# Kernel optimization log

Measured on AMD Instinct MI355X. Metric: run time of the kernel, lower is better.

## Reference

```python
import jax, jax.numpy as jnp
import numpy as np

EMB_DIM, D_H, BSZ, SEQ = 2048, 128, 4, 4096
HALF = D_H // 2


def apply_rope(x, sin, cos):
    # x: [b, s, d]; sin/cos: [s, d//2]; interleaved-pair rotation
    b, s, d = x.shape
    xr = x.reshape(b, s, d // 2, 2)
    x0, x1 = xr[..., 0], xr[..., 1]
    r0 = x0 * cos - x1 * sin
    r1 = x1 * cos + x0 * sin
    return jnp.stack([r0, r1], axis=-1).reshape(b, s, d)


def setup_inputs() -> dict:
    key = jax.random.key(0)
    kx, kq, kk, kv = jax.random.split(key, 4)
    x = jax.random.normal(kx, (BSZ, SEQ, EMB_DIM), dtype=jnp.float32)
    # causal mask (1 = attend, 0 = masked), matching mask[q,:] slicing in source
    mask = jnp.tril(jnp.ones((SEQ, SEQ), dtype=jnp.int32))
    # standard RoPE angle tables: [seq, d_h//2]
    inv_freq = 1.0 / (10000.0 ** (jnp.arange(HALF, dtype=jnp.float32) / HALF))
    angles = jnp.arange(SEQ, dtype=jnp.float32)[:, None] * inv_freq[None, :]
    sin, cos = jnp.sin(angles), jnp.cos(angles)
    scale = 1.0 / np.sqrt(EMB_DIM)
    W_Q = jax.random.normal(kq, (EMB_DIM, D_H), dtype=jnp.float32) * scale
    W_K = jax.random.normal(kk, (EMB_DIM, D_H), dtype=jnp.float32) * scale
    W_V = jax.random.normal(kv, (EMB_DIM, D_H), dtype=jnp.float32) * scale
    return {"x": x, "mask": mask, "sin": sin, "cos": cos,
            "W_Q": W_Q, "W_K": W_K, "W_V": W_V}


def reference(x, mask, sin, cos, W_Q, W_V, W_K):
    # QKV projections
    Q = apply_rope(x @ W_Q, sin, cos)  # [b, s, d_h]
    K = apply_rope(x @ W_K, sin, cos)  # [b, s, d_h]
    V = x @ W_V                        # [b, s, d_h]
    # The source's chunked loop is exactly full masked attention over all K/V.
    scores = jnp.einsum('bqd,bkd->bqk', Q, K) / jnp.sqrt(jnp.float32(D_H))
    scores = jnp.where(mask[None, :, :] == 0, -jnp.inf, scores)
    attn = jax.nn.softmax(scores, axis=-1)
    return jnp.einsum('bqk,bkd->bqd', attn, V)
```

## Files before the change

kernel.cpp:

```cpp
#include <hip/hip_runtime.h>
#include <stdint.h>
#include <stddef.h>

typedef __bf16 bf16;
typedef __bf16 bf16x8 __attribute__((ext_vector_type(8)));
typedef float f32x4 __attribute__((ext_vector_type(4)));
typedef unsigned int uint32x2 __attribute__((ext_vector_type(2)));
typedef unsigned int uint32x4 __attribute__((ext_vector_type(4)));

typedef const __attribute__((address_space(1))) uint32_t GU32;
typedef __attribute__((address_space(3))) uint32_t LU32;

__device__ __forceinline__ f32x4 mfma16(bf16x8 a, bf16x8 b, f32x4 c) {
  return __builtin_amdgcn_mfma_f32_16x16x32_bf16(a, b, c, 0, 0, 0);
}
__device__ __forceinline__ void gload16(const void* g, void* l) {
  __builtin_amdgcn_global_load_lds((GU32*)g, (LU32*)l, 16, 0, 0);
}

__global__ __launch_bounds__(256) void k_prep(const float* __restrict__ Wq,
                                              const float* __restrict__ Wk,
                                              const float* __restrict__ Wv,
                                              bf16* __restrict__ Wct) {
  __shared__ float tile[64][65];
  const int tid = threadIdx.x;
  const int widx = blockIdx.x >> 6, rem = blockIdx.x & 63;
  const int k0 = (rem >> 1) * 64, n0 = (rem & 1) * 64;
  const float* W = (widx == 0) ? Wq : (widx == 1) ? Wk : Wv;
  const int rg = tid >> 4, cq = tid & 15;
#pragma unroll
  for (int i = 0; i < 4; ++i) {
    int krow = i * 16 + rg;
    f32x4 v = *(const f32x4*)(W + (size_t)(k0 + krow) * 128 + n0 + cq * 4);
#pragma unroll
    for (int j = 0; j < 4; ++j) tile[krow][cq * 4 + j] = v[j];
  }
  __syncthreads();
#pragma unroll
  for (int i = 0; i < 4; ++i) {
    int nrow = i * 16 + rg;
    union { bf16 h[4]; uint32x2 u; } pk;
#pragma unroll
    for (int j = 0; j < 4; ++j) pk.h[j] = (bf16)tile[cq * 4 + j][nrow];
    *(uint32x2*)(Wct + (size_t)(widx * 128 + n0 + nrow) * 2048 + k0 + cq * 4) = pk.u;
  }
}

__global__ __launch_bounds__(512, 1) void k_proj(
    const float* __restrict__ x, const float* __restrict__ sint, const float* __restrict__ cost,
    const bf16* __restrict__ Wct, bf16* __restrict__ Qg, bf16* __restrict__ Kg,
    bf16* __restrict__ Vtg) {
  __shared__ __align__(16) uint8_t smem[114688];
  const int tid = threadIdx.x;
  const int lane = tid & 63, w = tid >> 6;
  const int l15 = lane & 15, l16 = lane >> 4;
  const int mb = blockIdx.x;
  const int arow = tid >> 3, aj = tid & 7;

  f32x4 acc[4][3] = {};
  f32x4 regA[2], regB[2];
  uint32x4 br[6];

  const float* abase = x + (size_t)(mb * 64 + arow) * 2048 + aj * 8;

  auto stageB_load = [&](int ks) {
    int k0 = ks * 64;
#pragma unroll
    for (int i = 0; i < 6; ++i) {
      int L = i * 8192 + tid * 16;
      int n = L >> 7, gp = (L >> 4) & 7;
      int cc = gp ^ (n & 7);
      br[i] = *(const uint32x4*)((const uint8_t*)Wct + (((size_t)n * 2048 + k0 + cc * 8) << 1));
    }
  };
  auto stageB_write = [&](int buf) {
    uint8_t* bbm = smem + 16384 + buf * 49152;
#pragma unroll
    for (int i = 0; i < 6; ++i)
      *(uint32x4*)(bbm + i * 8192 + tid * 16) = br[i];
  };
  auto loadA = [&](int ks, f32x4* r) {
    const f32x4* p = (const f32x4*)(abase + ks * 64);
    r[0] = p[0];
    r[1] = p[1];
  };
  auto writeA = [&](int buf, const f32x4* r) {
    uint8_t* ab = smem + buf * 8192;
    union { bf16 v[8]; uint32x4 u; } pk;
#pragma unroll
    for (int e = 0; e < 8; ++e) pk.v[e] = (bf16)r[e >> 2][e & 3];
    *(uint32x4*)(ab + arow * 128 + (((aj ^ (arow & 7)) & 7) << 4)) = pk.u;
  };
  auto compute = [&](int buf) {
    uint8_t* ab = smem + buf * 8192;
    uint8_t* bbm = smem + 16384 + buf * 49152;
    bf16x8 af[2][4], bv[2][3];
#pragma unroll
    for (int kk = 0; kk < 2; ++kk) {
#pragma unroll
      for (int mt = 0; mt < 4; ++mt) {
        int ml = mt * 16 + l15;
        af[kk][mt] = *(const bf16x8*)(ab + ml * 128 + (((kk * 4 + l16) ^ (ml & 7)) << 4));
      }
#pragma unroll
      for (int nt = 0; nt < 3; ++nt) {
        int nl = w * 48 + nt * 16 + l15;
        bv[kk][nt] = *(const bf16x8*)(bbm + nl * 128 + (((kk * 4 + l16) ^ (nl & 7)) << 4));
      }
    }
    __builtin_amdgcn_s_setprio(1);
#pragma unroll
    for (int kk = 0; kk < 2; ++kk)
#pragma unroll
      for (int mt = 0; mt < 4; ++mt)
#pragma unroll
        for (int nt = 0; nt < 3; ++nt)
          acc[mt][nt] = mfma16(af[kk][mt], bv[kk][nt], acc[mt][nt]);
    __builtin_amdgcn_s_setprio(0);
  };

  loadA(0, regA);
  stageB_load(0);
  loadA(1, regB);
  stageB_write(0);
  writeA(0, regA);
  __syncthreads();

  for (int ks = 0; ks < 32; ks += 2) {
    {
      if (ks + 1 < 32) stageB_load(ks + 1);
      if (ks + 2 < 32) loadA(ks + 2, regA);
      compute(0);
      if (ks + 1 < 32) { stageB_write(1); writeA(1, regB); }
      __syncthreads();
    }
    if (ks + 1 < 32) {
      if (ks + 2 < 32) { stageB_load(ks + 2); loadA(ks + 3, regB); }
      compute(1);
      if (ks + 2 < 32) { stageB_write(0); writeA(0, regA); }
      __syncthreads();
    }
  }

  const int bb = mb >> 6;
#pragma unroll
  for (int mt = 0; mt < 4; ++mt) {
    int gm = mb * 64 + mt * 16 + l16 * 4;
    int s0 = gm & 4095;
#pragma unroll
    for (int nt = 0; nt < 3; ++nt) {
      int jcol = w * 48 + nt * 16 + l15;
      f32x4 v = acc[mt][nt];
      if (jcol < 256) {
        int p = (jcol & 127) >> 1;
        bool even = ((jcol & 1) == 0);
#pragma unroll
        for (int r = 0; r < 4; ++r) {
          float pv = __shfl_xor(v[r], 1);
          int s = s0 + r;
          float cs = cost[s * 64 + p], sn = sint[s * 64 + p];
          float nv = even ? (v[r] * cs - pv * sn) : (v[r] * cs + pv * sn);
          bf16 hb = (bf16)nv;
          if (jcol < 128) Qg[((size_t)(bb << 12) + s) * 128 + jcol] = hb;
          else            Kg[((size_t)(bb << 12) + s) * 128 + jcol - 128] = hb;
        }
      } else {
        int d = jcol - 256;
        union { bf16 h[4]; uint32x2 u; } pk;
#pragma unroll
        for (int r = 0; r < 4; ++r) pk.h[r] = (bf16)v[r];
        *(uint32x2*)((uint8_t*)Vtg + (((size_t)(bb << 7) + d) * 4096 + s0) * 2) = pk.u;
      }
    }
  }
}

__global__ __launch_bounds__(256, 2) void k_attn(
    const bf16* __restrict__ Qg, const bf16* __restrict__ Kg, const bf16* __restrict__ Vtg,
    float* __restrict__ PO, float* __restrict__ ML) {
  __shared__ __align__(16) uint8_t smem[81920];
  const int tid = threadIdx.x;
  const int lane = tid & 63, w = tid >> 6;
  const int l15 = lane & 15, l16 = lane >> 4;

  int gid = blockIdx.x;
  int b = gid / 80, rr = gid % 80;
  int j, c;
  if (rr < 8)       { j = rr;                 c = 0; }
  else if (rr < 24) { j = 8 + ((rr - 8) >> 1);  c = (rr - 8) & 1; }
  else if (rr < 48) { j = 16 + (rr - 24) / 3;   c = (rr - 24) % 3; }
  else              { j = 24 + ((rr - 48) >> 2); c = (rr - 48) & 3; }

  const int q0w = j * 128 + w * 32;
  const int kv_lo = c * 1024;
  const int kv_hi = min((c + 1) * 1024, (j + 1) * 128);
  const int T = (kv_hi - kv_lo) >> 6;

  bf16x8 qf[2][4];
#pragma unroll
  for (int qt = 0; qt < 2; ++qt)
#pragma unroll
    for (int kk = 0; kk < 4; ++kk)
      qf[qt][kk] = *(const bf16x8*)(Qg + ((size_t)(b << 12) + q0w + qt * 16 + l15) * 128 + kk * 32 + l16 * 8);

  f32x4 o[2][8] = {};
  float m_r[2] = {-1e30f, -1e30f};
  float l_r[2] = {0.f, 0.f};
  uint8_t* pb = smem + 65536 + w * 4096;

  auto stage = [&](int t) {
    uint8_t* kb = smem + (t & 1) * 32768;
    uint8_t* vb = kb + 16384;
    int kv0 = kv_lo + t * 64;
#pragma unroll
    for (int i = 0; i < 4; ++i) {
      int L = i * 4096 + tid * 16;
      {
        int kv = L >> 8, cp = (L >> 4) & 15, cc = cp ^ (kv & 7);
        const uint8_t* src = (const uint8_t*)Kg + ((size_t)((b << 12) + kv0 + kv) << 8) + (cc << 4);
        gload16(src, kb + i * 4096 + w * 1024);
      }
      {
        int d = L >> 7, cp = (L >> 4) & 7, cc = cp ^ (d & 7);
        const uint8_t* src = (const uint8_t*)Vtg + ((size_t)(((b << 7) + d) << 12) + kv0 + (cc << 3)) * 2;
        gload16(src, vb + i * 4096 + w * 1024);
      }
    }
  };

  stage(0);
  __syncthreads();

  for (int t = 0; t < T; ++t) {
    if (t + 1 < T) stage(t + 1);
    const int kv0 = kv_lo + t * 64;
    if (kv0 <= q0w + 31) {
      uint8_t* kb = smem + (t & 1) * 32768;
      uint8_t* vb = kb + 16384;
      f32x4 sfr[4][2] = {};
#pragma unroll
      for (int kk = 0; kk < 4; ++kk) {
#pragma unroll
        for (int kvt = 0; kvt < 4; ++kvt) {
          int kvl = kvt * 16 + l15;
          bf16x8 kf = *(const bf16x8*)(kb + (kvl << 8) + (((kk * 4 + l16) ^ (kvl & 7)) << 4));
#pragma unroll
          for (int qt = 0; qt < 2; ++qt)
            sfr[kvt][qt] = mfma16(kf, qf[qt][kk], sfr[kvt][qt]);
        }
      }
      const bool need_mask = (kv0 + 63 > q0w);
      const float scale = 0.08838834764831845f;
#pragma unroll
      for (int qt = 0; qt < 2; ++qt) {
        const int q = q0w + qt * 16 + l15;
        float pvv[4][4];
        float tmax = -1e30f;
#pragma unroll
        for (int kvt = 0; kvt < 4; ++kvt)
#pragma unroll
          for (int r = 0; r < 4; ++r) {
            float sv = sfr[kvt][qt][r] * scale;
            if (need_mask) {
              int kv = kv0 + kvt * 16 + l16 * 4 + r;
              if (kv > q) sv = -1e30f;
            }
            pvv[kvt][r] = sv;
            tmax = fmaxf(tmax, sv);
          }
        tmax = fmaxf(tmax, __shfl_xor(tmax, 16));
        tmax = fmaxf(tmax, __shfl_xor(tmax, 32));
        float mnew = fmaxf(m_r[qt], tmax);
        float corr = __expf(m_r[qt] - mnew);
        m_r[qt] = mnew;
        float rs = 0.f;
#pragma unroll
        for (int kvt = 0; kvt < 4; ++kvt)
#pragma unroll
          for (int r = 0; r < 4; ++r) {
            float p = __expf(pvv[kvt][r] - mnew);
            pvv[kvt][r] = p;
            rs += p;
          }
        rs += __shfl_xor(rs, 16);
        rs += __shfl_xor(rs, 32);
        l_r[qt] = l_r[qt] * corr + rs;
        const int qrow = qt * 16 + l15;
#pragma unroll
        for (int kvt = 0; kvt < 4; ++kvt) {
          union { bf16 h[4]; uint32x2 u; } pk;
#pragma unroll
          for (int r = 0; r < 4; ++r) pk.h[r] = (bf16)pvv[kvt][r];
          int kv2 = kvt * 32 + l16 * 8;
          *(uint32x2*)(pb + qrow * 128 + ((((kv2 >> 4) ^ (qrow & 7)) << 4) | (kv2 & 15))) = pk.u;
        }
#pragma unroll
        for (int r = 0; r < 4; ++r) {
          float cr = __shfl(corr, l16 * 4 + r);
#pragma unroll
          for (int dt = 0; dt < 8; ++dt) o[qt][dt][r] *= cr;
        }
      }
#pragma unroll
      for (int kvb = 0; kvb < 2; ++kvb) {
        bf16x8 pa[2];
#pragma unroll
        for (int qt = 0; qt < 2; ++qt) {
          int qrow = qt * 16 + l15;
          int kv2 = kvb * 64 + l16 * 16;
          pa[qt] = *(const bf16x8*)(pb + qrow * 128 + (((kv2 >> 4) ^ (qrow & 7)) << 4));
        }
#pragma unroll
        for (int dt = 0; dt < 8; ++dt) {
          int d = dt * 16 + l15;
          bf16x8 vf = *(const bf16x8*)(vb + (d << 7) + (((kvb * 4 + l16) ^ (d & 7)) << 4));
#pragma unroll
          for (int qt = 0; qt < 2; ++qt)
            o[qt][dt] = mfma16(pa[qt], vf, o[qt][dt]);
        }
      }
    }
    __syncthreads();
  }

  float* POb = PO + (size_t)((b * 32 + j) * 4 + c) * 16384;
#pragma unroll
  for (int qt = 0; qt < 2; ++qt)
#pragma unroll
    for (int dt = 0; dt < 8; ++dt)
#pragma unroll
      for (int r = 0; r < 4; ++r)
        POb[(w * 32 + qt * 16 + l16 * 4 + r) * 128 + dt * 16 + l15] = o[qt][dt][r];
  float* MLb = ML + (size_t)((b * 32 + j) * 4 + c) * 256;
  if (l16 == 0) {
#pragma unroll
    for (int qt = 0; qt < 2; ++qt) {
      MLb[w * 32 + qt * 16 + l15] = m_r[qt];
      MLb[128 + w * 32 + qt * 16 + l15] = l_r[qt];
    }
  }
}

__global__ void k_combine(const float* __restrict__ PO, const float* __restrict__ ML,
                          float* __restrict__ out) {
  int blk = blockIdx.x;
  int b = blk >> 5, j = blk & 31;
  int nc = 1 + (j >> 3);
  int t = threadIdx.x;
  int q = t >> 1, half = t & 1;
  const float* MLb = ML + (size_t)(b * 32 + j) * 4 * 256;
  float mv[4], lv[4];
  float ms = -1e30f;
  for (int cc = 0; cc < nc; ++cc) {
    mv[cc] = MLb[cc * 256 + q];
    lv[cc] = MLb[cc * 256 + 128 + q];
    ms = fmaxf(ms, mv[cc]);
  }
  float wgt[4];
  float den = 0.f;
  for (int cc = 0; cc < nc; ++cc) { wgt[cc] = __expf(mv[cc] - ms); den += wgt[cc] * lv[cc]; }
  float inv = 1.f / den;
  const float* POb = PO + (size_t)(b * 32 + j) * 4 * 16384 + q * 128 + half * 64;
  float* ob = out + ((size_t)(b << 12) + j * 128 + q) * 128 + half * 64;
  for (int d = 0; d < 64; d += 4) {
    f32x4 a = {0.f, 0.f, 0.f, 0.f};
    for (int cc = 0; cc < nc; ++cc) {
      f32x4 v = *(const f32x4*)(POb + cc * 16384 + d);
      a += v * wgt[cc];
    }
    a *= inv;
    *(f32x4*)(ob + d) = a;
  }
}

extern "C" void kernel_launch(void* const* d_in, const int* in_sizes, int n_in,
                              void* d_out, int out_size, void* d_ws, size_t ws_size,
                              hipStream_t stream) {
  const float* x = (const float*)d_in[0];
  const float* sint = (const float*)d_in[2];
  const float* cost = (const float*)d_in[3];
  const float* Wq = (const float*)d_in[4];
  const float* Wk = (const float*)d_in[5];
  const float* Wv = (const float*)d_in[6];
  uint8_t* ws = (uint8_t*)d_ws;

  bf16* Wct = (bf16*)(ws + 0x0);
  bf16* Qg  = (bf16*)(ws + 0x180000);
  bf16* Kg  = (bf16*)(ws + 0x580000);
  bf16* Vtg = (bf16*)(ws + 0x980000);
  float* PO = (float*)(ws + 0xD80000);
  float* ML = (float*)(ws + 0x2D80000);
  float* out = (float*)d_out;

  hipLaunchKernelGGL(k_prep, dim3(192), dim3(256), 0, stream, Wq, Wk, Wv, Wct);
  hipLaunchKernelGGL(k_proj, dim3(256), dim3(512), 0, stream, x, sint, cost, Wct, Qg, Kg, Vtg);
  hipLaunchKernelGGL(k_attn, dim3(320), dim3(256), 0, stream, Qg, Kg, Vtg, PO, ML);
  hipLaunchKernelGGL(k_combine, dim3(128), dim3(256), 0, stream, PO, ML, out);
}
```

Before: 130.6 us.

## Use 512-thread attention blocks over 256 query rows and write unsplit tiles directly

The attention kernel now handles 256 query rows per block with 8 waves, so each staged K/V tile is shared by twice as many queries. The grid shrinks from 320 to 160 blocks and the KV split scheme is rescaled to match. Blocks that cover a query tile in a single KV chunk normalize their result and write it straight to the output, so the combine kernel only runs on the 48 split tiles. In exchange, LDS per block and waves per block go up while there are fewer blocks to spread over the CUs, which can hurt occupancy and load balance.

```diff
diff --git a/kernel.cpp b/kernel.cpp
--- a/kernel.cpp
+++ b/kernel.cpp
@@ -175,25 +175,26 @@
   }
 }
 
-__global__ __launch_bounds__(256, 2) void k_attn(
+__global__ __launch_bounds__(512, 1) void k_attn(
     const bf16* __restrict__ Qg, const bf16* __restrict__ Kg, const bf16* __restrict__ Vtg,
-    float* __restrict__ PO, float* __restrict__ ML) {
-  __shared__ __align__(16) uint8_t smem[81920];
+    float* __restrict__ PO, float* __restrict__ ML, float* __restrict__ out) {
+  __shared__ __align__(16) uint8_t smem[98304];
   const int tid = threadIdx.x;
   const int lane = tid & 63, w = tid >> 6;
   const int l15 = lane & 15, l16 = lane >> 4;
 
   int gid = blockIdx.x;
-  int b = gid / 80, rr = gid % 80;
-  int j, c;
-  if (rr < 8)       { j = rr;                 c = 0; }
-  else if (rr < 24) { j = 8 + ((rr - 8) >> 1);  c = (rr - 8) & 1; }
-  else if (rr < 48) { j = 16 + (rr - 24) / 3;   c = (rr - 24) % 3; }
-  else              { j = 24 + ((rr - 48) >> 2); c = (rr - 48) & 3; }
-
-  const int q0w = j * 128 + w * 32;
+  int b = gid / 40, rr = gid % 40;
+  int jp, c;
+  if (rr < 4)       { jp = rr;                 c = 0; }
+  else if (rr < 12) { jp = 4 + ((rr - 4) >> 1);  c = (rr - 4) & 1; }
+  else if (rr < 24) { jp = 8 + (rr - 12) / 3;    c = (rr - 12) % 3; }
+  else              { jp = 12 + ((rr - 24) >> 2); c = (rr - 24) & 3; }
+  const bool single = (jp < 4);
+
+  const int q0w = jp * 256 + w * 32;
   const int kv_lo = c * 1024;
-  const int kv_hi = min((c + 1) * 1024, (j + 1) * 128);
+  const int kv_hi = min((c + 1) * 1024, (jp + 1) * 256);
   const int T = (kv_hi - kv_lo) >> 6;
 
   bf16x8 qf[2][4];
@@ -213,17 +214,17 @@
     uint8_t* vb = kb + 16384;
     int kv0 = kv_lo + t * 64;
 #pragma unroll
-    for (int i = 0; i < 4; ++i) {
-      int L = i * 4096 + tid * 16;
+    for (int i = 0; i < 2; ++i) {
+      int L = i * 8192 + tid * 16;
       {
         int kv = L >> 8, cp = (L >> 4) & 15, cc = cp ^ (kv & 7);
         const uint8_t* src = (const uint8_t*)Kg + ((size_t)((b << 12) + kv0 + kv) << 8) + (cc << 4);
-        gload16(src, kb + i * 4096 + w * 1024);
+        gload16(src, kb + L);
       }
       {
         int d = L >> 7, cp = (L >> 4) & 7, cc = cp ^ (d & 7);
         const uint8_t* src = (const uint8_t*)Vtg + ((size_t)(((b << 7) + d) << 12) + kv0 + (cc << 3)) * 2;
-        gload16(src, vb + i * 4096 + w * 1024);
+        gload16(src, vb + L);
       }
     }
   };
@@ -323,49 +324,65 @@
     __syncthreads();
   }
 
-  float* POb = PO + (size_t)((b * 32 + j) * 4 + c) * 16384;
-#pragma unroll
-  for (int qt = 0; qt < 2; ++qt)
-#pragma unroll
-    for (int dt = 0; dt < 8; ++dt)
-#pragma unroll
-      for (int r = 0; r < 4; ++r)
-        POb[(w * 32 + qt * 16 + l16 * 4 + r) * 128 + dt * 16 + l15] = o[qt][dt][r];
-  float* MLb = ML + (size_t)((b * 32 + j) * 4 + c) * 256;
-  if (l16 == 0) {
+  if (single) {
 #pragma unroll
     for (int qt = 0; qt < 2; ++qt) {
-      MLb[w * 32 + qt * 16 + l15] = m_r[qt];
-      MLb[128 + w * 32 + qt * 16 + l15] = l_r[qt];
-    }
-  }
-}
-
-__global__ void k_combine(const float* __restrict__ PO, const float* __restrict__ ML,
-                          float* __restrict__ out) {
+#pragma unroll
+      for (int r = 0; r < 4; ++r) {
+        float li = __shfl(l_r[qt], l16 * 4 + r);
+        float inv = 1.0f / li;
+        size_t row = (size_t)(b << 12) + q0w + qt * 16 + l16 * 4 + r;
+#pragma unroll
+        for (int dt = 0; dt < 8; ++dt)
+          out[row * 128 + dt * 16 + l15] = o[qt][dt][r] * inv;
+      }
+    }
+  } else {
+    float* POb = PO + (size_t)((b * 16 + jp) * 4 + c) * 32768;
+#pragma unroll
+    for (int qt = 0; qt < 2; ++qt)
+#pragma unroll
+      for (int dt = 0; dt < 8; ++dt)
+#pragma unroll
+        for (int r = 0; r < 4; ++r)
+          POb[(w * 32 + qt * 16 + l16 * 4 + r) * 128 + dt * 16 + l15] = o[qt][dt][r];
+    float* MLb = ML + (size_t)((b * 16 + jp) * 4 + c) * 512;
+    if (l16 == 0) {
+#pragma unroll
+      for (int qt = 0; qt < 2; ++qt) {
+        MLb[w * 32 + qt * 16 + l15] = m_r[qt];
+        MLb[256 + w * 32 + qt * 16 + l15] = l_r[qt];
+      }
+    }
+  }
+}
+
+__global__ __launch_bounds__(512) void k_combine(const float* __restrict__ PO,
+                                                 const float* __restrict__ ML,
+                                                 float* __restrict__ out) {
   int blk = blockIdx.x;
-  int b = blk >> 5, j = blk & 31;
-  int nc = 1 + (j >> 3);
+  int b = blk / 12, jp = blk % 12 + 4;
+  int nc = 1 + (jp >> 2);
   int t = threadIdx.x;
   int q = t >> 1, half = t & 1;
-  const float* MLb = ML + (size_t)(b * 32 + j) * 4 * 256;
+  const float* MLb = ML + (size_t)((b * 16 + jp) * 4) * 512;
   float mv[4], lv[4];
   float ms = -1e30f;
   for (int cc = 0; cc < nc; ++cc) {
-    mv[cc] = MLb[cc * 256 + q];
-    lv[cc] = MLb[cc * 256 + 128 + q];
+    mv[cc] = MLb[cc * 512 + q];
+    lv[cc] = MLb[cc * 512 + 256 + q];
     ms = fmaxf(ms, mv[cc]);
   }
   float wgt[4];
   float den = 0.f;
   for (int cc = 0; cc < nc; ++cc) { wgt[cc] = __expf(mv[cc] - ms); den += wgt[cc] * lv[cc]; }
   float inv = 1.f / den;
-  const float* POb = PO + (size_t)(b * 32 + j) * 4 * 16384 + q * 128 + half * 64;
-  float* ob = out + ((size_t)(b << 12) + j * 128 + q) * 128 + half * 64;
+  const float* POb = PO + (size_t)((b * 16 + jp) * 4) * 32768 + q * 128 + half * 64;
+  float* ob = out + ((size_t)(b << 12) + jp * 256 + q) * 128 + half * 64;
   for (int d = 0; d < 64; d += 4) {
     f32x4 a = {0.f, 0.f, 0.f, 0.f};
     for (int cc = 0; cc < nc; ++cc) {
-      f32x4 v = *(const f32x4*)(POb + cc * 16384 + d);
+      f32x4 v = *(const f32x4*)(POb + cc * 32768 + d);
       a += v * wgt[cc];
     }
     a *= inv;
@@ -394,6 +411,6 @@
 
   hipLaunchKernelGGL(k_prep, dim3(192), dim3(256), 0, stream, Wq, Wk, Wv, Wct);
   hipLaunchKernelGGL(k_proj, dim3(256), dim3(512), 0, stream, x, sint, cost, Wct, Qg, Kg, Vtg);
-  hipLaunchKernelGGL(k_attn, dim3(320), dim3(256), 0, stream, Qg, Kg, Vtg, PO, ML);
-  hipLaunchKernelGGL(k_combine, dim3(128), dim3(256), 0, stream, PO, ML, out);
-}
+  hipLaunchKernelGGL(k_attn, dim3(160), dim3(512), 0, stream, Qg, Kg, Vtg, PO, ML, out);
+  hipLaunchKernelGGL(k_combine, dim3(48), dim3(512), 0, stream, PO, ML, out);
+}
```

Result: slower. 136.1 us (+4.2%).
